# Kernel optimization log

Hardware: AMD Instinct MI355X
Metric: run time of the kernel (lower is better)

The kernel has to match this reference:

```python
import jax, jax.numpy as jnp
import numpy as np

N = 8192        # total nodes (64 graphs x 128 nodes)
B = 64          # graphs in batch
E0 = 32768      # explicit edges (self-loops added in forward)
IN = 32         # input node feats
H = [64, 64]    # hidden feats per NNConv layer
BOND = 5        # bond (edge) feature dim, hard-coded in source


def setup_inputs() -> dict:
    key = jax.random.key(0)
    ks = jax.random.split(key, 16)
    s = 0.1
    node_feats = jax.random.normal(ks[0], (N, IN), jnp.float32)
    edge_feats = jax.random.normal(ks[1], (E0, BOND), jnp.float32)
    src = jax.random.randint(ks[2], (E0,), 0, N)
    dst = jax.random.randint(ks[3], (E0,), 0, N)
    graph_ids = jnp.repeat(jnp.arange(B), N // B)  # contiguous batched graphs
    timestep = jax.random.randint(ks[4], (B, 1), 0, 1000).astype(jnp.float32)
    # NNConv layer 1: edge MLP Linear(BOND, IN*H0) + output bias
    edge_W1 = jax.random.normal(ks[5], (BOND, IN * H[0]), jnp.float32) * s
    edge_b1 = jax.random.normal(ks[6], (IN * H[0],), jnp.float32) * s
    bias1 = jax.random.normal(ks[7], (H[0],), jnp.float32) * s
    # NNConv layer 2: edge MLP Linear(BOND, H0*H1) + output bias
    edge_W2 = jax.random.normal(ks[8], (BOND, H[0] * H[1]), jnp.float32) * s
    edge_b2 = jax.random.normal(ks[9], (H[0] * H[1],), jnp.float32) * s
    bias2 = jax.random.normal(ks[10], (H[1],), jnp.float32) * s
    # WeightAndSum pooling: Linear(H1, 1) + sigmoid
    ws_W = jax.random.normal(ks[11], (H[1], 1), jnp.float32) * s
    ws_b = jax.random.normal(ks[12], (1,), jnp.float32) * s
    return {
        "node_feats": node_feats, "edge_feats": edge_feats,
        "src": src, "dst": dst, "graph_ids": graph_ids, "timestep": timestep,
        "edge_W1": edge_W1, "edge_b1": edge_b1, "bias1": bias1,
        "edge_W2": edge_W2, "edge_b2": edge_b2, "bias2": bias2,
        "ws_W": ws_W, "ws_b": ws_b,
    }


def _nnconv(h, ef, src, dst, edge_W, edge_b, bias, din, dout):
    # edge MLP -> per-edge weight matrix [E, din, dout]
    W = (ef @ edge_W + edge_b).reshape(-1, din, dout)
    # gather source feats, per-edge matmul, scatter-sum to destinations
    m = jnp.einsum('ei,eio->eo', h[src], W)
    agg = jax.ops.segment_sum(m, dst, num_segments=N)
    return agg + bias


def reference(node_feats, edge_feats, src, dst, graph_ids, timestep,
              edge_W1, edge_b1, bias1, edge_W2, edge_b2, bias2, ws_W, ws_b):
    # add self-loops with zero edge features (forward does dgl.add_self_loop)
    loop = jnp.arange(N)
    src_a = jnp.concatenate([src, loop])
    dst_a = jnp.concatenate([dst, loop])
    ef = jnp.concatenate([edge_feats, jnp.zeros((N, BOND), edge_feats.dtype)])

    h = jax.nn.relu(_nnconv(node_feats, ef, src_a, dst_a, edge_W1, edge_b1, bias1, IN, H[0]))
    h = jax.nn.relu(_nnconv(h, ef, src_a, dst_a, edge_W2, edge_b2, bias2, H[0], H[1]))

    # WeightAndSum pooling + max pooling per graph
    w = jax.nn.sigmoid(h @ ws_W + ws_b)                     # [N,1]
    g_sum = jax.ops.segment_sum(h * w, graph_ids, num_segments=B)
    g_max = jax.ops.segment_max(h, graph_ids, num_segments=B)
    graph_feats = jnp.concatenate([g_sum, g_max], axis=1)    # [B, 2*H1]

    # sinusoidal timestep conditioning (channels = 2*H1 = 128)
    C = 2 * H[-1]
    inv_freq = 1.0 / (10000.0 ** (jnp.arange(0, C, 2).astype(jnp.float32) / C))
    arg = timestep * inv_freq                                # [B, C//2]
    pos_enc = jnp.concatenate([jnp.sin(arg), jnp.cos(arg)], axis=-1)
    graph_feats = graph_feats + pos_enc

    return jnp.tanh(jax.nn.relu(graph_feats))
```

## Files before the change

kernel.cpp:

```cpp
#include <hip/hip_runtime.h>
#include <math.h>

#define N_NODES 8192
#define NEDGE   32768
#define BGRAPH  64

template <int DIN>
__global__ __launch_bounds__(384) void transform_kernel(
    const float* __restrict__ h_in,
    const float* __restrict__ edge_W,
    const float* __restrict__ edge_b,
    const float* __restrict__ bias,
    float* __restrict__ TS,
    float* __restrict__ agg,
    int relu_in) {
  __shared__ float hTile[16][DIN];
  const int n0 = blockIdx.x * 16;

  for (int idx = threadIdx.x; idx < 16 * DIN; idx += 384) {
    float v = h_in[(size_t)n0 * DIN + idx];
    if (relu_in) v = fmaxf(v, 0.0f);
    hTile[idx / DIN][idx % DIN] = v;
  }
  __syncthreads();

  const int j = threadIdx.x;
  const int o = j & 63;
  const bool isS = (j >= 320);
  const float* wsrc = isS ? (edge_b + o)
                          : (edge_W + (size_t)(j >> 6) * (DIN * 64) + o);
  float wcol[DIN];
#pragma unroll
  for (int i = 0; i < DIN; ++i) wcol[i] = wsrc[(size_t)i * 64];
  const float bo = bias[o];

  for (int n = 0; n < 16; ++n) {
    float acc = 0.0f;
#pragma unroll
    for (int i = 0; i < DIN; ++i) acc = fmaf(hTile[n][i], wcol[i], acc);
    TS[(size_t)(n0 + n) * 384 + j] = acc;
    if (isS) agg[(size_t)(n0 + n) * 64 + o] = acc + bo;
  }
}

__global__ __launch_bounds__(256) void edge_kernel(
    const float* __restrict__ ef,
    const int* __restrict__ src,
    const int* __restrict__ dst,
    const float* __restrict__ TS,
    float* __restrict__ agg) {
  const int e = (blockIdx.x * 256 + threadIdx.x) >> 6;
  const int o = threadIdx.x & 63;
  if (e >= NEDGE) return;

  const int s = src[e];
  const int d = dst[e];
  const float c0 = ef[(size_t)e * 5 + 0];
  const float c1 = ef[(size_t)e * 5 + 1];
  const float c2 = ef[(size_t)e * 5 + 2];
  const float c3 = ef[(size_t)e * 5 + 3];
  const float c4 = ef[(size_t)e * 5 + 4];

  const float* row = TS + (size_t)s * 384;
  float m = row[320 + o];
  m = fmaf(c0, row[o], m);
  m = fmaf(c1, row[64 + o], m);
  m = fmaf(c2, row[128 + o], m);
  m = fmaf(c3, row[192 + o], m);
  m = fmaf(c4, row[256 + o], m);

  atomicAdd(&agg[(size_t)d * 64 + o], m);
}

__global__ __launch_bounds__(256) void pool_kernel(
    const float* __restrict__ agg2,
    const float* __restrict__ ws_W,
    const float* __restrict__ ws_b,
    const float* __restrict__ timestep,
    float* __restrict__ out) {
  __shared__ float tile[128][65];
  __shared__ float wn[128];
  __shared__ float partS[4][64];
  __shared__ float partM[4][64];
  __shared__ float wsw[64];

  const int g = blockIdx.x;
  const int t = threadIdx.x;

  const float* base = agg2 + (size_t)g * 128 * 64;
  for (int idx = t; idx < 128 * 64; idx += 256) {
    tile[idx >> 6][idx & 63] = fmaxf(base[idx], 0.0f);
  }
  if (t < 64) wsw[t] = ws_W[t];
  __syncthreads();

  if (t < 128) {
    float acc = ws_b[0];
    for (int o = 0; o < 64; ++o) acc = fmaf(tile[t][o], wsw[o], acc);
    wn[t] = 1.0f / (1.0f + expf(-acc));
  }
  __syncthreads();

  const int o = t & 63;
  const int q = t >> 6;
  float s = 0.0f, mx = 0.0f;
  for (int n = q * 32; n < q * 32 + 32; ++n) {
    const float v = tile[n][o];
    s = fmaf(v, wn[n], s);
    mx = fmaxf(mx, v);
  }
  partS[q][o] = s;
  partM[q][o] = mx;
  __syncthreads();

  if (t < 128) {
    const int c = t;
    const int oo = c & 63;
    float val;
    if (c < 64) {
      val = partS[0][oo] + partS[1][oo] + partS[2][oo] + partS[3][oo];
    } else {
      val = fmaxf(fmaxf(partM[0][oo], partM[1][oo]),
                  fmaxf(partM[2][oo], partM[3][oo]));
    }
    const float invf = exp2f(-(float)oo * (13.287712379549449f / 64.0f));
    const float ang = timestep[g] * invf;
    const float pe = (c < 64) ? sinf(ang) : cosf(ang);
    out[(size_t)g * 128 + c] = tanhf(fmaxf(val + pe, 0.0f));
  }
}

extern "C" void kernel_launch(void* const* d_in, const int* in_sizes, int n_in,
                              void* d_out, int out_size, void* d_ws, size_t ws_size,
                              hipStream_t stream) {
  const float* node_feats = (const float*)d_in[0];
  const float* edge_feats = (const float*)d_in[1];
  const int*   src        = (const int*)d_in[2];
  const int*   dst        = (const int*)d_in[3];
  const float* timestep   = (const float*)d_in[5];
  const float* edge_W1    = (const float*)d_in[6];
  const float* edge_b1    = (const float*)d_in[7];
  const float* bias1      = (const float*)d_in[8];
  const float* edge_W2    = (const float*)d_in[9];
  const float* edge_b2    = (const float*)d_in[10];
  const float* bias2      = (const float*)d_in[11];
  const float* ws_W       = (const float*)d_in[12];
  const float* ws_b       = (const float*)d_in[13];
  float* out = (float*)d_out;

  float* TS   = (float*)d_ws;
  float* agg1 = TS + (size_t)N_NODES * 384;
  float* agg2 = agg1 + (size_t)N_NODES * 64;

  transform_kernel<32><<<N_NODES / 16, 384, 0, stream>>>(
      node_feats, edge_W1, edge_b1, bias1, TS, agg1, 0);
  edge_kernel<<<NEDGE / 4, 256, 0, stream>>>(edge_feats, src, dst, TS, agg1);
  transform_kernel<64><<<N_NODES / 16, 384, 0, stream>>>(
      agg1, edge_W2, edge_b2, bias2, TS, agg2, 1);
  edge_kernel<<<NEDGE / 4, 256, 0, stream>>>(edge_feats, src, dst, TS, agg2);
  pool_kernel<<<BGRAPH, 256, 0, stream>>>(agg2, ws_W, ws_b, timestep, out);
}
```

Baseline: 142.0 us.

## Fuse all stages into one persistent cooperative kernel with grid syncs

Replaces five separate launches with a single cooperative persistent kernel that runs both transforms, both edge passes and the pooling in sequence, separated by grid-wide barriers. Blocks loop over tiles, edges and graphs with grid-stride loops, and shared memory is shared between phases through a union. The aim is to remove launch gaps and per-kernel ramp-up. In exchange the grid is capped by occupancy, so edge-phase parallelism is reduced and each grid.sync adds cost. A fallback keeps the multi-kernel path if the cooperative launch fails.

```diff
diff --git a/kernel.cpp b/kernel.cpp
--- a/kernel.cpp
+++ b/kernel.cpp
@@ -1,29 +1,31 @@
 #include <hip/hip_runtime.h>
+#include <hip/hip_cooperative_groups.h>
 #include <math.h>
+
+namespace cg = cooperative_groups;
 
 #define N_NODES 8192
 #define NEDGE   32768
 #define BGRAPH  64
+#define NTHR    384
+#define NTILES  512
+
+union Smem {
+  float h[16 * 64];
+  struct {
+    float tile[128][65];
+    float wn[128];
+    float partS[4][64];
+    float partM[4][64];
+    float wsw[64];
+  } pool;
+};
 
 template <int DIN>
-__global__ __launch_bounds__(384) void transform_kernel(
-    const float* __restrict__ h_in,
-    const float* __restrict__ edge_W,
-    const float* __restrict__ edge_b,
-    const float* __restrict__ bias,
-    float* __restrict__ TS,
-    float* __restrict__ agg,
-    int relu_in) {
-  __shared__ float hTile[16][DIN];
-  const int n0 = blockIdx.x * 16;
-
-  for (int idx = threadIdx.x; idx < 16 * DIN; idx += 384) {
-    float v = h_in[(size_t)n0 * DIN + idx];
-    if (relu_in) v = fmaxf(v, 0.0f);
-    hTile[idx / DIN][idx % DIN] = v;
-  }
-  __syncthreads();
-
+__device__ __forceinline__ void transform_tiles(
+    Smem& sm, const float* __restrict__ h_in, const float* __restrict__ edge_W,
+    const float* __restrict__ edge_b, const float* __restrict__ bias,
+    float* __restrict__ TS, float* __restrict__ agg, int relu_in) {
   const int j = threadIdx.x;
   const int o = j & 63;
   const bool isS = (j >= 320);
@@ -34,105 +36,151 @@
   for (int i = 0; i < DIN; ++i) wcol[i] = wsrc[(size_t)i * 64];
   const float bo = bias[o];
 
-  for (int n = 0; n < 16; ++n) {
-    float acc = 0.0f;
+  for (int tile = blockIdx.x; tile < NTILES; tile += gridDim.x) {
+    const int n0 = tile * 16;
+    for (int idx = threadIdx.x; idx < 16 * DIN; idx += NTHR) {
+      float v = h_in[(size_t)n0 * DIN + idx];
+      if (relu_in) v = fmaxf(v, 0.0f);
+      sm.h[idx] = v;
+    }
+    __syncthreads();
+    for (int n = 0; n < 16; ++n) {
+      const float* hr = &sm.h[n * DIN];
+      float acc = 0.0f;
 #pragma unroll
-    for (int i = 0; i < DIN; ++i) acc = fmaf(hTile[n][i], wcol[i], acc);
-    TS[(size_t)(n0 + n) * 384 + j] = acc;
-    if (isS) agg[(size_t)(n0 + n) * 64 + o] = acc + bo;
-  }
+      for (int i = 0; i < DIN; ++i) acc = fmaf(hr[i], wcol[i], acc);
+      TS[(size_t)(n0 + n) * 384 + j] = acc;
+      if (isS) agg[(size_t)(n0 + n) * 64 + o] = acc + bo;
+    }
+    __syncthreads();
+  }
+}
+
+__device__ __forceinline__ void edge_pass(
+    const float* __restrict__ ef, const int* __restrict__ src,
+    const int* __restrict__ dst, const float* __restrict__ TS,
+    float* __restrict__ agg) {
+  const int nw = (gridDim.x * blockDim.x) >> 6;
+  const int w  = (blockIdx.x * blockDim.x + threadIdx.x) >> 6;
+  const int o  = threadIdx.x & 63;
+  for (int e = w; e < NEDGE; e += nw) {
+    const int s = src[e];
+    const int d = dst[e];
+    const float c0 = ef[(size_t)e * 5 + 0];
+    const float c1 = ef[(size_t)e * 5 + 1];
+    const float c2 = ef[(size_t)e * 5 + 2];
+    const float c3 = ef[(size_t)e * 5 + 3];
+    const float c4 = ef[(size_t)e * 5 + 4];
+    const float* row = TS + (size_t)s * 384;
+    float m = row[320 + o];
+    m = fmaf(c0, row[o], m);
+    m = fmaf(c1, row[64 + o], m);
+    m = fmaf(c2, row[128 + o], m);
+    m = fmaf(c3, row[192 + o], m);
+    m = fmaf(c4, row[256 + o], m);
+    atomicAdd(&agg[(size_t)d * 64 + o], m);
+  }
+}
+
+__device__ __forceinline__ void pool_graphs(
+    Smem& sm, const float* __restrict__ agg2, const float* __restrict__ ws_W,
+    const float* __restrict__ ws_b, const float* __restrict__ timestep,
+    float* __restrict__ out) {
+  const int t = threadIdx.x;
+  for (int g = blockIdx.x; g < BGRAPH; g += gridDim.x) {
+    const float* base = agg2 + (size_t)g * 128 * 64;
+    for (int idx = t; idx < 128 * 64; idx += NTHR)
+      sm.pool.tile[idx >> 6][idx & 63] = fmaxf(base[idx], 0.0f);
+    if (t < 64) sm.pool.wsw[t] = ws_W[t];
+    __syncthreads();
+    if (t < 128) {
+      float acc = ws_b[0];
+      for (int o = 0; o < 64; ++o)
+        acc = fmaf(sm.pool.tile[t][o], sm.pool.wsw[o], acc);
+      sm.pool.wn[t] = 1.0f / (1.0f + expf(-acc));
+    }
+    __syncthreads();
+    if (t < 256) {
+      const int o = t & 63, q = t >> 6;
+      float s = 0.0f, mx = 0.0f;
+      for (int n = q * 32; n < q * 32 + 32; ++n) {
+        const float v = sm.pool.tile[n][o];
+        s = fmaf(v, sm.pool.wn[n], s);
+        mx = fmaxf(mx, v);
+      }
+      sm.pool.partS[q][o] = s;
+      sm.pool.partM[q][o] = mx;
+    }
+    __syncthreads();
+    if (t < 128) {
+      const int c = t, oo = c & 63;
+      float val;
+      if (c < 64)
+        val = sm.pool.partS[0][oo] + sm.pool.partS[1][oo] +
+              sm.pool.partS[2][oo] + sm.pool.partS[3][oo];
+      else
+        val = fmaxf(fmaxf(sm.pool.partM[0][oo], sm.pool.partM[1][oo]),
+                    fmaxf(sm.pool.partM[2][oo], sm.pool.partM[3][oo]));
+      const float invf = exp2f(-(float)oo * (13.287712379549449f / 64.0f));
+      const float ang = timestep[g] * invf;
+      const float pe = (c < 64) ? sinf(ang) : cosf(ang);
+      out[(size_t)g * 128 + c] = tanhf(fmaxf(val + pe, 0.0f));
+    }
+    __syncthreads();
+  }
+}
+
+__global__ __launch_bounds__(NTHR, 3) void fused_gcn(
+    const float* __restrict__ node_feats, const float* __restrict__ edge_feats,
+    const int* __restrict__ src, const int* __restrict__ dst,
+    const float* __restrict__ timestep, const float* __restrict__ edge_W1,
+    const float* __restrict__ edge_b1, const float* __restrict__ bias1,
+    const float* __restrict__ edge_W2, const float* __restrict__ edge_b2,
+    const float* __restrict__ bias2, const float* __restrict__ ws_W,
+    const float* __restrict__ ws_b, float* __restrict__ TS,
+    float* __restrict__ agg1, float* __restrict__ agg2,
+    float* __restrict__ out) {
+  __shared__ Smem sm;
+  cg::grid_group grid = cg::this_grid();
+
+  transform_tiles<32>(sm, node_feats, edge_W1, edge_b1, bias1, TS, agg1, 0);
+  grid.sync();
+  edge_pass(edge_feats, src, dst, TS, agg1);
+  grid.sync();
+  transform_tiles<64>(sm, agg1, edge_W2, edge_b2, bias2, TS, agg2, 1);
+  grid.sync();
+  edge_pass(edge_feats, src, dst, TS, agg2);
+  grid.sync();
+  pool_graphs(sm, agg2, ws_W, ws_b, timestep, out);
+}
+
+template <int DIN>
+__global__ __launch_bounds__(NTHR) void transform_kernel(
+    const float* __restrict__ h_in, const float* __restrict__ edge_W,
+    const float* __restrict__ edge_b, const float* __restrict__ bias,
+    float* __restrict__ TS, float* __restrict__ agg, int relu_in) {
+  __shared__ Smem sm;
+  transform_tiles<DIN>(sm, h_in, edge_W, edge_b, bias, TS, agg, relu_in);
 }
 
 __global__ __launch_bounds__(256) void edge_kernel(
-    const float* __restrict__ ef,
-    const int* __restrict__ src,
-    const int* __restrict__ dst,
-    const float* __restrict__ TS,
+    const float* __restrict__ ef, const int* __restrict__ src,
+    const int* __restrict__ dst, const float* __restrict__ TS,
     float* __restrict__ agg) {
-  const int e = (blockIdx.x * 256 + threadIdx.x) >> 6;
-  const int o = threadIdx.x & 63;
-  if (e >= NEDGE) return;
-
-  const int s = src[e];
-  const int d = dst[e];
-  const float c0 = ef[(size_t)e * 5 + 0];
-  const float c1 = ef[(size_t)e * 5 + 1];
-  const float c2 = ef[(size_t)e * 5 + 2];
-  const float c3 = ef[(size_t)e * 5 + 3];
-  const float c4 = ef[(size_t)e * 5 + 4];
-
-  const float* row = TS + (size_t)s * 384;
-  float m = row[320 + o];
-  m = fmaf(c0, row[o], m);
-  m = fmaf(c1, row[64 + o], m);
-  m = fmaf(c2, row[128 + o], m);
-  m = fmaf(c3, row[192 + o], m);
-  m = fmaf(c4, row[256 + o], m);
-
-  atomicAdd(&agg[(size_t)d * 64 + o], m);
-}
-
-__global__ __launch_bounds__(256) void pool_kernel(
-    const float* __restrict__ agg2,
-    const float* __restrict__ ws_W,
-    const float* __restrict__ ws_b,
-    const float* __restrict__ timestep,
+  edge_pass(ef, src, dst, TS, agg);
+}
+
+__global__ __launch_bounds__(NTHR) void pool_kernel(
+    const float* __restrict__ agg2, const float* __restrict__ ws_W,
+    const float* __restrict__ ws_b, const float* __restrict__ timestep,
     float* __restrict__ out) {
-  __shared__ float tile[128][65];
-  __shared__ float wn[128];
-  __shared__ float partS[4][64];
-  __shared__ float partM[4][64];
-  __shared__ float wsw[64];
-
-  const int g = blockIdx.x;
-  const int t = threadIdx.x;
-
-  const float* base = agg2 + (size_t)g * 128 * 64;
-  for (int idx = t; idx < 128 * 64; idx += 256) {
-    tile[idx >> 6][idx & 63] = fmaxf(base[idx], 0.0f);
-  }
-  if (t < 64) wsw[t] = ws_W[t];
-  __syncthreads();
-
-  if (t < 128) {
-    float acc = ws_b[0];
-    for (int o = 0; o < 64; ++o) acc = fmaf(tile[t][o], wsw[o], acc);
-    wn[t] = 1.0f / (1.0f + expf(-acc));
-  }
-  __syncthreads();
-
-  const int o = t & 63;
-  const int q = t >> 6;
-  float s = 0.0f, mx = 0.0f;
-  for (int n = q * 32; n < q * 32 + 32; ++n) {
-    const float v = tile[n][o];
-    s = fmaf(v, wn[n], s);
-    mx = fmaxf(mx, v);
-  }
-  partS[q][o] = s;
-  partM[q][o] = mx;
-  __syncthreads();
-
-  if (t < 128) {
-    const int c = t;
-    const int oo = c & 63;
-    float val;
-    if (c < 64) {
-      val = partS[0][oo] + partS[1][oo] + partS[2][oo] + partS[3][oo];
-    } else {
-      val = fmaxf(fmaxf(partM[0][oo], partM[1][oo]),
-                  fmaxf(partM[2][oo], partM[3][oo]));
-    }
-    const float invf = exp2f(-(float)oo * (13.287712379549449f / 64.0f));
-    const float ang = timestep[g] * invf;
-    const float pe = (c < 64) ? sinf(ang) : cosf(ang);
-    out[(size_t)g * 128 + c] = tanhf(fmaxf(val + pe, 0.0f));
-  }
+  __shared__ Smem sm;
+  pool_graphs(sm, agg2, ws_W, ws_b, timestep, out);
 }
 
 extern "C" void kernel_launch(void* const* d_in, const int* in_sizes, int n_in,
-                              void* d_out, int out_size, void* d_ws, size_t ws_size,
-                              hipStream_t stream) {
+                              void* d_out, int out_size, void* d_ws,
+                              size_t ws_size, hipStream_t stream) {
   const float* node_feats = (const float*)d_in[0];
   const float* edge_feats = (const float*)d_in[1];
   const int*   src        = (const int*)d_in[2];
@@ -152,11 +200,39 @@
   float* agg1 = TS + (size_t)N_NODES * 384;
   float* agg2 = agg1 + (size_t)N_NODES * 64;
 
-  transform_kernel<32><<<N_NODES / 16, 384, 0, stream>>>(
-      node_feats, edge_W1, edge_b1, bias1, TS, agg1, 0);
-  edge_kernel<<<NEDGE / 4, 256, 0, stream>>>(edge_feats, src, dst, TS, agg1);
-  transform_kernel<64><<<N_NODES / 16, 384, 0, stream>>>(
-      agg1, edge_W2, edge_b2, bias2, TS, agg2, 1);
-  edge_kernel<<<NEDGE / 4, 256, 0, stream>>>(edge_feats, src, dst, TS, agg2);
-  pool_kernel<<<BGRAPH, 256, 0, stream>>>(agg2, ws_W, ws_b, timestep, out);
-}
+  static int coop_grid = -2;
+  if (coop_grid == -2) {
+    int maxB = 0;
+    if (hipOccupancyMaxActiveBlocksPerMultiprocessor(
+            &maxB, (const void*)fused_gcn, NTHR, 0) == hipSuccess &&
+        maxB > 0) {
+      coop_grid = maxB * 256;
+      if (coop_grid > NTILES) coop_grid = NTILES;
+    } else {
+      coop_grid = -1;
+    }
+  }
+
+  bool launched = false;
+  if (coop_grid > 0) {
+    void* args[] = {&node_feats, &edge_feats, &src,     &dst,     &timestep,
+                    &edge_W1,    &edge_b1,    &bias1,   &edge_W2, &edge_b2,
+                    &bias2,      &ws_W,       &ws_b,    &TS,      &agg1,
+                    &agg2,       &out};
+    if (hipLaunchCooperativeKernel((const void*)fused_gcn, dim3(coop_grid),
+                                   dim3(NTHR), args, 0, stream) == hipSuccess)
+      launched = true;
+    else
+      coop_grid = -1;
+  }
+
+  if (!launched) {
+    transform_kernel<32><<<NTILES, NTHR, 0, stream>>>(
+        node_feats, edge_W1, edge_b1, bias1, TS, agg1, 0);
+    edge_kernel<<<NEDGE / 4, 256, 0, stream>>>(edge_feats, src, dst, TS, agg1);
+    transform_kernel<64><<<NTILES, NTHR, 0, stream>>>(
+        agg1, edge_W2, edge_b2, bias2, TS, agg2, 1);
+    edge_kernel<<<NEDGE / 4, 256, 0, stream>>>(edge_feats, src, dst, TS, agg2);
+    pool_kernel<<<BGRAPH, NTHR, 0, stream>>>(agg2, ws_W, ws_b, timestep, out);
+  }
+}
```

Result: slower. 146.9 us (+3.4%).

## Replace atomic scatter edge kernels with CSR-by-destination pull aggregation

Applied to the files above, without the earlier changes.

Builds a destination-sorted CSR (count, scan, fill) once per call, packing each edge's features and source index into a 32-byte record. The two atomic-scatter edge kernels become pull kernels, one wavefront per node, that sum incoming messages in registers and write agg once, folding in the self-loop term and bias. This removes float atomics and the separate agg init stores. In exchange it adds four small launches including a single-block scan, and the pull loop is serial per node with uneven degrees. Pool loads are also vectorised to float4.

```diff
diff --git a/kernel.cpp b/kernel.cpp
--- a/kernel.cpp
+++ b/kernel.cpp
@@ -4,15 +4,15 @@
 #define N_NODES 8192
 #define NEDGE   32768
 #define BGRAPH  64
+#define NTILES  512
+
 
 template <int DIN>
 __global__ __launch_bounds__(384) void transform_kernel(
     const float* __restrict__ h_in,
     const float* __restrict__ edge_W,
     const float* __restrict__ edge_b,
-    const float* __restrict__ bias,
     float* __restrict__ TS,
-    float* __restrict__ agg,
     int relu_in) {
   __shared__ float hTile[16][DIN];
   const int n0 = blockIdx.x * 16;
@@ -26,50 +26,106 @@
 
   const int j = threadIdx.x;
   const int o = j & 63;
-  const bool isS = (j >= 320);
-  const float* wsrc = isS ? (edge_b + o)
-                          : (edge_W + (size_t)(j >> 6) * (DIN * 64) + o);
+  const float* wsrc = (j >= 320) ? (edge_b + o)
+                                 : (edge_W + (size_t)(j >> 6) * (DIN * 64) + o);
   float wcol[DIN];
 #pragma unroll
   for (int i = 0; i < DIN; ++i) wcol[i] = wsrc[(size_t)i * 64];
-  const float bo = bias[o];
 
   for (int n = 0; n < 16; ++n) {
     float acc = 0.0f;
 #pragma unroll
     for (int i = 0; i < DIN; ++i) acc = fmaf(hTile[n][i], wcol[i], acc);
     TS[(size_t)(n0 + n) * 384 + j] = acc;
-    if (isS) agg[(size_t)(n0 + n) * 64 + o] = acc + bo;
-  }
-}
-
-__global__ __launch_bounds__(256) void edge_kernel(
-    const float* __restrict__ ef,
-    const int* __restrict__ src,
-    const int* __restrict__ dst,
+  }
+}
+
+__global__ __launch_bounds__(256) void csr_count(const int* __restrict__ dst,
+                                                 int* __restrict__ deg) {
+  const int e = blockIdx.x * 256 + threadIdx.x;
+  if (e < NEDGE) atomicAdd(&deg[dst[e]], 1);
+}
+
+__global__ __launch_bounds__(1024) void csr_scan(const int* __restrict__ deg,
+                                                 int* __restrict__ row_off,
+                                                 int* __restrict__ cursor) {
+  __shared__ int part[1024];
+  const int t = threadIdx.x;
+  int loc[8];
+  int sum = 0;
+#pragma unroll
+  for (int j = 0; j < 8; ++j) {
+    loc[j] = sum;
+    sum += deg[t * 8 + j];
+  }
+  part[t] = sum;
+  __syncthreads();
+  for (int off = 1; off < 1024; off <<= 1) {
+    const int add = (t >= off) ? part[t - off] : 0;
+    __syncthreads();
+    part[t] += add;
+    __syncthreads();
+  }
+  const int base = (t == 0) ? 0 : part[t - 1];
+#pragma unroll
+  for (int j = 0; j < 8; ++j) {
+    const int v = base + loc[j];
+    row_off[t * 8 + j] = v;
+    cursor[t * 8 + j] = v;
+  }
+  if (t == 1023) row_off[N_NODES] = part[1023];
+}
+
+__global__ __launch_bounds__(256) void csr_fill(
+    const int* __restrict__ src, const int* __restrict__ dst,
+    const float* __restrict__ ef, int* __restrict__ cursor,
+    float* __restrict__ rec) {
+  const int e = blockIdx.x * 256 + threadIdx.x;
+  if (e >= NEDGE) return;
+  const int pos = atomicAdd(&cursor[dst[e]], 1);
+  const float4 a = make_float4(ef[(size_t)e * 5 + 0], ef[(size_t)e * 5 + 1],
+                               ef[(size_t)e * 5 + 2], ef[(size_t)e * 5 + 3]);
+  const float4 b = make_float4(ef[(size_t)e * 5 + 4],
+                               __int_as_float(src[e]), 0.0f, 0.0f);
+  ((float4*)rec)[2 * pos + 0] = a;
+  ((float4*)rec)[2 * pos + 1] = b;
+}
+
+__global__ __launch_bounds__(256) void pull_kernel(
+    const float* __restrict__ rec,
+    const int* __restrict__ row_off,
     const float* __restrict__ TS,
+    const float* __restrict__ bias,
     float* __restrict__ agg) {
-  const int e = (blockIdx.x * 256 + threadIdx.x) >> 6;
+  const int n = (blockIdx.x * 256 + threadIdx.x) >> 6;
   const int o = threadIdx.x & 63;
-  if (e >= NEDGE) return;
-
-  const int s = src[e];
-  const int d = dst[e];
-  const float c0 = ef[(size_t)e * 5 + 0];
-  const float c1 = ef[(size_t)e * 5 + 1];
-  const float c2 = ef[(size_t)e * 5 + 2];
-  const float c3 = ef[(size_t)e * 5 + 3];
-  const float c4 = ef[(size_t)e * 5 + 4];
-
-  const float* row = TS + (size_t)s * 384;
-  float m = row[320 + o];
-  m = fmaf(c0, row[o], m);
-  m = fmaf(c1, row[64 + o], m);
-  m = fmaf(c2, row[128 + o], m);
-  m = fmaf(c3, row[192 + o], m);
-  m = fmaf(c4, row[256 + o], m);
-
-  atomicAdd(&agg[(size_t)d * 64 + o], m);
+  const int r0 = row_off[n];
+  const int r1 = row_off[n + 1];
+
+  float acc = TS[(size_t)n * 384 + 320 + o] + bias[o];
+
+  float4 ra, rb;
+  if (r0 < r1) {
+    ra = ((const float4*)rec)[2 * r0 + 0];
+    rb = ((const float4*)rec)[2 * r0 + 1];
+  }
+  for (int k = r0; k < r1; ++k) {
+    const float c0 = ra.x, c1 = ra.y, c2 = ra.z, c3 = ra.w, c4 = rb.x;
+    const int s = __float_as_int(rb.y);
+    if (k + 1 < r1) {
+      ra = ((const float4*)rec)[2 * (k + 1) + 0];
+      rb = ((const float4*)rec)[2 * (k + 1) + 1];
+    }
+    const float* row = TS + (size_t)s * 384;
+    float m = row[320 + o];
+    m = fmaf(c0, row[o], m);
+    m = fmaf(c1, row[64 + o], m);
+    m = fmaf(c2, row[128 + o], m);
+    m = fmaf(c3, row[192 + o], m);
+    m = fmaf(c4, row[256 + o], m);
+    acc += m;
+  }
+  agg[(size_t)n * 64 + o] = acc;
 }
 
 __global__ __launch_bounds__(256) void pool_kernel(
@@ -87,9 +143,15 @@
   const int g = blockIdx.x;
   const int t = threadIdx.x;
 
-  const float* base = agg2 + (size_t)g * 128 * 64;
-  for (int idx = t; idx < 128 * 64; idx += 256) {
-    tile[idx >> 6][idx & 63] = fmaxf(base[idx], 0.0f);
+  const float4* base4 = (const float4*)(agg2 + (size_t)g * 128 * 64);
+  for (int i4 = t; i4 < 128 * 16; i4 += 256) {
+    const float4 v = base4[i4];
+    const int n = i4 >> 4;
+    const int c = (i4 & 15) * 4;
+    tile[n][c + 0] = fmaxf(v.x, 0.0f);
+    tile[n][c + 1] = fmaxf(v.y, 0.0f);
+    tile[n][c + 2] = fmaxf(v.z, 0.0f);
+    tile[n][c + 3] = fmaxf(v.w, 0.0f);
   }
   if (t < 64) wsw[t] = ws_W[t];
   __syncthreads();
@@ -131,8 +193,8 @@
 }
 
 extern "C" void kernel_launch(void* const* d_in, const int* in_sizes, int n_in,
-                              void* d_out, int out_size, void* d_ws, size_t ws_size,
-                              hipStream_t stream) {
+                              void* d_out, int out_size, void* d_ws,
+                              size_t ws_size, hipStream_t stream) {
   const float* node_feats = (const float*)d_in[0];
   const float* edge_feats = (const float*)d_in[1];
   const int*   src        = (const int*)d_in[2];
@@ -148,15 +210,26 @@
   const float* ws_b       = (const float*)d_in[13];
   float* out = (float*)d_out;
 
-  float* TS   = (float*)d_ws;
-  float* agg1 = TS + (size_t)N_NODES * 384;
-  float* agg2 = agg1 + (size_t)N_NODES * 64;
-
-  transform_kernel<32><<<N_NODES / 16, 384, 0, stream>>>(
-      node_feats, edge_W1, edge_b1, bias1, TS, agg1, 0);
-  edge_kernel<<<NEDGE / 4, 256, 0, stream>>>(edge_feats, src, dst, TS, agg1);
-  transform_kernel<64><<<N_NODES / 16, 384, 0, stream>>>(
-      agg1, edge_W2, edge_b2, bias2, TS, agg2, 1);
-  edge_kernel<<<NEDGE / 4, 256, 0, stream>>>(edge_feats, src, dst, TS, agg2);
+  float* TS     = (float*)d_ws;
+  float* agg1   = TS + (size_t)N_NODES * 384;
+  float* agg2   = agg1 + (size_t)N_NODES * 64;
+  float* rec    = agg2 + (size_t)N_NODES * 64;
+  int*   deg    = (int*)(rec + (size_t)NEDGE * 8);
+  int*   rowoff = deg + N_NODES;
+  int*   cursor = rowoff + N_NODES + 8;
+
+  hipMemsetAsync(deg, 0, N_NODES * sizeof(int), stream);
+  csr_count<<<NEDGE / 256, 256, 0, stream>>>(dst, deg);
+  csr_scan<<<1, 1024, 0, stream>>>(deg, rowoff, cursor);
+  csr_fill<<<NEDGE / 256, 256, 0, stream>>>(src, dst, edge_feats, cursor, rec);
+
+  transform_kernel<32><<<NTILES, 384, 0, stream>>>(
+      node_feats, edge_W1, edge_b1, TS, 0);
+  pull_kernel<<<N_NODES / 4, 256, 0, stream>>>(rec, rowoff, TS, bias1, agg1);
+
+  transform_kernel<64><<<NTILES, 384, 0, stream>>>(
+      agg1, edge_W2, edge_b2, TS, 1);
+  pull_kernel<<<N_NODES / 4, 256, 0, stream>>>(rec, rowoff, TS, bias2, agg2);
+
   pool_kernel<<<BGRAPH, 256, 0, stream>>>(agg2, ws_W, ws_b, timestep, out);
 }
```

New measurement: 155.5 us. 9.5% more time.
